# Optimization experiments

Hardware: AMD Instinct MI355X
Metric: run time of the kernel (lower is better)

The kernel has to match this reference:

```python
import jax, jax.numpy as jnp
from jax import lax
import numpy as np

NUM_KIND = 4
V, H, B = 34, 32, 4096   # raw vertical (2 rows dropped), horizontal, batch
KS = 33                  # odd-rounded max(V-2, H)
NUM_DEPTH = 4
N_SQ = 100


def _conv(x, w):
    # x: (N,1,h,w), w: (1,1,KS,KS); torch Conv2d == cross-correlation == lax default
    return lax.conv_general_dilated(x, w, (1, 1), 'SAME',
                                    dimension_numbers=('NCHW', 'OIHW', 'NCHW'))


def _conv_k(x, w):
    # x: (K,B,1,h,w) -> conv each map with the shared 1-channel kernel
    k, b, c, h, wd = x.shape
    return _conv(x.reshape(k * b, c, h, wd), w).reshape(k, b, c, h, wd)


def setup_inputs() -> dict:
    key = jax.random.key(0)
    ks = jax.random.split(key, 8)
    std = 0.3
    return {
        'dots':    jax.random.randint(ks[0], (V, H, B), 0, NUM_KIND + 1, dtype=jnp.int32),
        'w_each':  jax.random.normal(ks[1], (1, 1, KS, KS), jnp.float32) * std,
        'w_not':   jax.random.normal(ks[2], (1, 1, KS, KS), jnp.float32) * std,
        'w_not2':  jax.random.normal(ks[3], (1, 1, KS, KS), jnp.float32) * std,
        'w_empty': jax.random.normal(ks[4], (1, 1, KS, KS), jnp.float32) * std,
        'W1':      jax.random.normal(ks[5], (N_SQ, (V - 2) * H), jnp.float32) * std,
        'W2':      jax.random.normal(ks[6], (N_SQ, N_SQ), jnp.float32) * std,
        'W3':      jax.random.normal(ks[7], (1, N_SQ), jnp.float32) * std,
    }


def reference(dots, w_each, w_not, w_not2, w_empty, W1, W2, W3):
    # drop last 2 vertical rows, layout (V-2,H,B) -> (B,1,V-2,H)
    board = dots[:-2].astype(jnp.float32).transpose(2, 0, 1)[:, None]  # (B,1,h,w)

    empty = (board == 0).astype(jnp.float32)
    E = _conv(empty, w_empty)                                           # (B,1,h,w)

    kinds = jnp.arange(1, NUM_KIND + 1, dtype=board.dtype).reshape(NUM_KIND, 1, 1, 1, 1)
    each = (board[None] == kinds).astype(jnp.float32)                   # (K,B,1,h,w)
    notm = ((each + empty[None]) == 0).astype(jnp.float32)              # (K,B,1,h,w)

    # first pass: per-color value, masked to that color's cells
    notm_conv = _conv_k(notm, w_not)      # note: the torch code LOGS the convolved not-mask
    v = _conv_k(each, w_each) + E[None] - notm_conv
    L = each * v                          # each_color_value_log (masked)
    s = jax.nn.sigmoid(L.sum(axis=0))     # all_color_value_2nd, (B,1,h,w)

    # iterative diffusion; torch mutates the log in-place each depth:
    # L <- mask * (L + E + conv2nd(notm_conv * before)); before is detached
    for _ in range(NUM_DEPTH):
        before = lax.stop_gradient(s)
        C = _conv_k(notm_conv * before[None], w_not2)
        L = each * (L + E[None] + C)
        s = jax.nn.sigmoid(L.sum(axis=0))

    feat = s.reshape(s.shape[0], -1)      # (B, (V-2)*H)
    x = jax.nn.leaky_relu(feat @ W1.T, 0.2)
    x = jax.nn.leaky_relu(x @ W2.T, 0.2)
    return x @ W3.T                        # (B,1)
```

## Files before the change

kernel.cpp:

```cpp
#include <hip/hip_runtime.h>
#include <cstdint>
#include <cstddef>


typedef _Float16 f16;
typedef __attribute__((ext_vector_type(8))) _Float16 f16x8;
typedef __attribute__((ext_vector_type(4))) float f32x4;

#define NB   4096
#define PIX  1024
#define MR   (NB * 4)

__device__ __forceinline__ void gld_lds16(const void* g, void* l) {
    __builtin_amdgcn_global_load_lds(
        (const __attribute__((address_space(1))) void*)g,
        (__attribute__((address_space(3))) void*)l, 16, 0, 0);
}

__global__ void build_all(const float* __restrict__ we, const float* __restrict__ wn,
                          const float* __restrict__ wn2, const float* __restrict__ wem,
                          const float* __restrict__ W1, const int* __restrict__ dots,
                          f16* __restrict__ Me, f16* __restrict__ Mn,
                          f16* __restrict__ Mn2, f16* __restrict__ Mem,
                          f16* __restrict__ W1b, unsigned char* __restrict__ board) {
    __shared__ unsigned char tile[64][68];
    int bi = blockIdx.x, t = threadIdx.x;
    if (bi < 4096) {
        int idx = bi * 256 + t;
        int o = idx >> 10, in = idx & 1023;
        int i = o >> 5, j = o & 31, a = in >> 5, b = in & 31;
        int u = a - i + 16, v = b - j + 16;
        bool ok = (u >= 0) && (u < 33) && (v >= 0) && (v < 33);
        int w = u * 33 + v;
        float ve = 0.f, vn = 0.f, vn2 = 0.f, vem = 0.f;
        if (ok) { ve = we[w]; vn = wn[w]; vn2 = wn2[w]; vem = wem[w]; }
        Me[idx]  = (f16)ve;
        Mn[idx]  = (f16)vn;
        Mn2[idx] = (f16)vn2;
        Mem[idx] = (f16)vem;
    } else if (bi < 4608) {
        int idx = (bi - 4096) * 256 + t;
        int j = idx >> 10, i = idx & 1023;
        W1b[idx] = (f16)(j < 100 ? W1[j * 1024 + i] : 0.f);
    } else {
        int bb = bi - 4608;
        int bp = bb & 15, bn = bb >> 4;
        int p0 = bp * 64, n0 = bn * 64;
        int ln = t & 63, lp = t >> 6;
#pragma unroll
        for (int j = 0; j < 16; j++) {
            int p = lp * 16 + j;
            tile[p][ln] = (unsigned char)dots[(size_t)(p0 + p) * 4096 + n0 + ln];
        }
        __syncthreads();
#pragma unroll
        for (int j = 0; j < 16; j++) {
            int n = lp * 16 + j;
            board[(size_t)(n0 + n) * 1024 + p0 + ln] = tile[ln][n];
        }
    }
}

__global__ void mk_sa(const f16* __restrict__ S1sel, const f16* __restrict__ En,
                      const f16* __restrict__ NC,
                      const unsigned char* __restrict__ board,
                      f16* __restrict__ Lsel, f16* __restrict__ P1) {
    int idx = blockIdx.x * 256 + threadIdx.x;
    int n = idx >> 10, o = idx & 1023;
    int c = board[idx];
    size_t r0 = (size_t)(4 * n) * PIX + o;
    f16 nc0 = NC[r0], nc1 = NC[r0 + PIX], nc2 = NC[r0 + 2 * PIX], nc3 = NC[r0 + 3 * PIX];
    float L = 0.f;
    if (c > 0) {
        float ncsel = (float)((c == 1) ? nc0 : (c == 2) ? nc1 : (c == 3) ? nc2 : nc3);
        L = (float)S1sel[idx] + (float)En[idx] - ncsel;
    }
    Lsel[idx] = (f16)L;
    f16 s = (f16)(1.f / (1.f + __expf(-L)));
    P1[r0]           = nc0 * s;
    P1[r0 + PIX]     = nc1 * s;
    P1[r0 + 2 * PIX] = nc2 * s;
    P1[r0 + 3 * PIX] = nc3 * s;
}

template <int MODE, int ASRC>
__device__ __forceinline__ void run_gemm(
    int bjob, int ypx, int nx, char* smem,
    const f16* __restrict__ X, const f16* __restrict__ B,
    const unsigned char* __restrict__ board,
    f16* __restrict__ outB, int ldo) {
    char* smB = smem;
    char* smA = smem + 16384;

    const int tid = threadIdx.x;
    const int wv = tid >> 6, ln = tid & 63;
    const int wm = wv >> 1, wn_ = wv & 1;
    const int lr = ln & 15, lq = ln >> 4;

    int xcd = bjob & 7, slot = bjob >> 3;
    int bx = slot % nx;
    int by = xcd * ypx + slot / nx;
    const int rtile = by * 128, otile = bx * 128;
    const int img0 = (ASRC == 4) ? rtile : (rtile >> 2);

    const f32x4 fz = {0.f, 0.f, 0.f, 0.f};
    f32x4 acc[4][4];
#pragma unroll
    for (int i = 0; i < 4; i++)
#pragma unroll
        for (int j = 0; j < 4; j++) acc[i][j] = fz;

    for (int kb = 0; kb < 1024; kb += 64) {
#pragma unroll
        for (int t = 0; t < 4; t++) {
            int c = (wv * 4 + t) * 64 + ln;
            int row = c >> 3, gcol = (c & 7) ^ (row & 7);
            gld_lds16(B + (size_t)(otile + row) * 1024 + kb + gcol * 8, smB + c * 16);
        }
        if (ASRC == 0) {
#pragma unroll
            for (int t = 0; t < 4; t++) {
                int c = (wv * 4 + t) * 64 + ln;
                int row = c >> 3, gcol = (c & 7) ^ (row & 7);
                gld_lds16(X + (size_t)(rtile + row) * 1024 + kb + gcol * 8, smA + c * 16);
            }
        } else if (ASRC == 4) {
#pragma unroll
            for (int t = 0; t < 2; t++) {
                int c = t * 256 + wv * 64 + ln;
                int row = c >> 2, g = (c & 3) ^ (row & 3);
                gld_lds16(board + (size_t)(img0 + row) * 1024 + kb + g * 16, smA + c * 16);
            }
        } else {
            if (wv < 2) {
                int c = wv * 64 + ln;
                int row = c >> 2, g = (c & 3) ^ (row & 3);
                gld_lds16(board + (size_t)(img0 + row) * 1024 + kb + g * 16, smA + c * 16);
            }
        }
        __syncthreads();

#pragma unroll
        for (int kk = 0; kk < 2; kk++) {
            const int oct = kk * 4 + lq;
            f16x8 af[4], bfr[4];
#pragma unroll
            for (int i = 0; i < 4; i++) {
                int rrow = wm * 64 + i * 16 + lr;
                if (ASRC == 0) {
                    af[i] = *(const f16x8*)(smA + rrow * 128 + (oct ^ (rrow & 7)) * 16);
                } else {
                    int m = (ASRC == 4) ? rrow : (rrow >> 2);
                    int k1 = (rrow & 3) + 1;
                    uint64_t bb = *(const uint64_t*)(smA + m * 64 +
                                    ((oct >> 1) ^ (m & 3)) * 16 + (oct & 1) * 8);
                    f16x8 v;
#pragma unroll
                    for (int jj = 0; jj < 8; jj++) {
                        int bj = (int)((bb >> (8 * jj)) & 0xff);
                        bool on = (ASRC == 2) ? (bj == k1)
                                : (ASRC == 3) ? (bj != 0 && bj != k1)
                                              : (bj == 0);
                        v[jj] = on ? (f16)1.f : (f16)0.f;
                    }
                    af[i] = v;
                }
            }
#pragma unroll
            for (int j = 0; j < 4; j++) {
                int brow = wn_ * 64 + j * 16 + lr;
                bfr[j] = *(const f16x8*)(smB + brow * 128 + (oct ^ (brow & 7)) * 16);
            }
#pragma unroll
            for (int i = 0; i < 4; i++)
#pragma unroll
                for (int j = 0; j < 4; j++)
                    acc[i][j] = __builtin_amdgcn_mfma_f32_16x16x32_f16(
                        af[i], bfr[j], acc[i][j], 0, 0, 0);
        }
        __syncthreads();
    }

#pragma unroll
    for (int i = 0; i < 4; i++) {
        int rbase = rtile + wm * 64 + i * 16 + lq * 4;
#pragma unroll
        for (int j = 0; j < 4; j++) {
            int o = otile + wn_ * 64 + j * 16 + lr;
            f32x4 a = acc[i][j];
            if (MODE == 0) {
#pragma unroll
                for (int v = 0; v < 4; v++)
                    outB[(size_t)(rbase + v) * ldo + o] = (f16)a[v];
            } else {
                int n = rbase >> 2;
                size_t no = (size_t)n * PIX + o;
                int c = board[no];
                float asel = (c == 1) ? a[0] : (c == 2) ? a[1] : (c == 3) ? a[2] : a[3];
                outB[no] = (f16)asel;
            }
        }
    }
}

__global__ void __launch_bounds__(256, 4) gemm_fa(
    const f16* __restrict__ Me, const f16* __restrict__ Mn,
    const f16* __restrict__ Mem, const unsigned char* __restrict__ board,
    f16* __restrict__ S1sel, f16* __restrict__ NC, f16* __restrict__ En) {
    __shared__ __attribute__((aligned(16))) char smem[24576];
    int bi = blockIdx.x;
    if (bi < 1024) {
        run_gemm<1, 2>(bi, 16, 8, smem, nullptr, Me, board, S1sel, 0);
    } else if (bi < 2048) {
        run_gemm<0, 3>(bi - 1024, 16, 8, smem, nullptr, Mn, board, NC, PIX);
    } else {
        run_gemm<0, 4>(bi - 2048, 4, 8, smem, nullptr, Mem, board, En, PIX);
    }
}

template <int MODE>
__global__ void __launch_bounds__(256, 2) gemm_depth(
    const f16* __restrict__ Pin, const f16* __restrict__ Mn2,
    const unsigned char* __restrict__ board, const f16* __restrict__ NC,
    const f16* __restrict__ En, f16* __restrict__ Lsel,
    f16* __restrict__ Pout, f16* __restrict__ feat) {
    __shared__ __attribute__((aligned(16))) char smem[32768];
    char* smB = smem;
    char* smA = smem + 16384;

    const int tid = threadIdx.x;
    const int wv = tid >> 6, ln = tid & 63;
    const int wm = wv >> 1, wn_ = wv & 1;
    const int lr = ln & 15, lq = ln >> 4;

    int bi = blockIdx.x;
    int xcd = bi & 7, slot = bi >> 3;
    int bx = slot & 7;
    int by = xcd * 16 + (slot >> 3);
    const int rtile = by * 128, otile = bx * 128;

    const f32x4 fz = {0.f, 0.f, 0.f, 0.f};
    f32x4 acc[4][4];
#pragma unroll
    for (int i = 0; i < 4; i++)
#pragma unroll
        for (int j = 0; j < 4; j++) acc[i][j] = fz;

    for (int kb = 0; kb < 1024; kb += 64) {
#pragma unroll
        for (int t = 0; t < 4; t++) {
            int c = (wv * 4 + t) * 64 + ln;
            int row = c >> 3, gcol = (c & 7) ^ (row & 7);
            gld_lds16(Mn2 + (size_t)(otile + row) * 1024 + kb + gcol * 8, smB + c * 16);
            gld_lds16(Pin + (size_t)(rtile + row) * 1024 + kb + gcol * 8, smA + c * 16);
        }
        __syncthreads();

#pragma unroll
        for (int kk = 0; kk < 2; kk++) {
            const int oct = kk * 4 + lq;
            f16x8 af[4], bfr[4];
#pragma unroll
            for (int i = 0; i < 4; i++) {
                int rrow = wm * 64 + i * 16 + lr;
                af[i] = *(const f16x8*)(smA + rrow * 128 + (oct ^ (rrow & 7)) * 16);
            }
#pragma unroll
            for (int j = 0; j < 4; j++) {
                int brow = wn_ * 64 + j * 16 + lr;
                bfr[j] = *(const f16x8*)(smB + brow * 128 + (oct ^ (brow & 7)) * 16);
            }
#pragma unroll
            for (int i = 0; i < 4; i++)
#pragma unroll
                for (int j = 0; j < 4; j++)
                    acc[i][j] = __builtin_amdgcn_mfma_f32_16x16x32_f16(
                        af[i], bfr[j], acc[i][j], 0, 0, 0);
        }
        __syncthreads();
    }

#pragma unroll
    for (int i = 0; i < 4; i++) {
        int rbase = rtile + wm * 64 + i * 16 + lq * 4;
#pragma unroll
        for (int j = 0; j < 4; j++) {
            int o = otile + wn_ * 64 + j * 16 + lr;
            f32x4 a = acc[i][j];
            int n = rbase >> 2;
            size_t no = (size_t)n * PIX + o;
            int c = board[no];
            float asel = (c == 1) ? a[0] : (c == 2) ? a[1] : (c == 3) ? a[2] : a[3];
            float E = (float)En[no];
            float Lnew = (c > 0) ? ((float)Lsel[no] + E + asel) : 0.f;
            float s = 1.f / (1.f + __expf(-Lnew));
            if (MODE == 4) {
                feat[no] = (f16)s;
            } else {
                Lsel[no] = (f16)Lnew;
                f16 sh = (f16)s;
                size_t r0 = (size_t)rbase * PIX + o;
                Pout[r0]           = NC[r0] * sh;
                Pout[r0 + PIX]     = NC[r0 + PIX] * sh;
                Pout[r0 + 2 * PIX] = NC[r0 + 2 * PIX] * sh;
                Pout[r0 + 3 * PIX] = NC[r0 + 3 * PIX] * sh;
            }
        }
    }
}

__global__ void __launch_bounds__(256) gemm_mlp_fused(
    const f16* __restrict__ feat, const f16* __restrict__ W1b,
    const float* __restrict__ W2, const float* __restrict__ W3,
    float* __restrict__ out) {
    __shared__ __attribute__((aligned(16))) char smem[47360];
    char* smB = smem;
    char* smA = smem + 16384;

    const int tid = threadIdx.x;
    const int wv = tid >> 6, ln = tid & 63;
    const int wm = wv >> 1, wn_ = wv & 1;
    const int lr = ln & 15, lq = ln >> 4;
    const int rtile = blockIdx.x * 128;

    const f32x4 fz = {0.f, 0.f, 0.f, 0.f};
    f32x4 acc[4][4];
#pragma unroll
    for (int i = 0; i < 4; i++)
#pragma unroll
        for (int j = 0; j < 4; j++) acc[i][j] = fz;

    for (int kb = 0; kb < 1024; kb += 64) {
#pragma unroll
        for (int t = 0; t < 4; t++) {
            int c = (wv * 4 + t) * 64 + ln;
            int row = c >> 3, gcol = (c & 7) ^ (row & 7);
            gld_lds16(W1b  + (size_t)row * 1024 + kb + gcol * 8, smB + c * 16);
            gld_lds16(feat + (size_t)(rtile + row) * 1024 + kb + gcol * 8, smA + c * 16);
        }
        __syncthreads();
#pragma unroll
        for (int kk = 0; kk < 2; kk++) {
            const int oct = kk * 4 + lq;
            f16x8 af[4], bfr[4];
#pragma unroll
            for (int i = 0; i < 4; i++) {
                int rrow = wm * 64 + i * 16 + lr;
                af[i] = *(const f16x8*)(smA + rrow * 128 + (oct ^ (rrow & 7)) * 16);
            }
#pragma unroll
            for (int j = 0; j < 4; j++) {
                int brow = wn_ * 64 + j * 16 + lr;
                bfr[j] = *(const f16x8*)(smB + brow * 128 + (oct ^ (brow & 7)) * 16);
            }
#pragma unroll
            for (int i = 0; i < 4; i++)
#pragma unroll
                for (int j = 0; j < 4; j++)
                    acc[i][j] = __builtin_amdgcn_mfma_f32_16x16x32_f16(
                        af[i], bfr[j], acc[i][j], 0, 0, 0);
        }
        __syncthreads();
    }

    float* xs  = (float*)smem;
    f16*   sW2 = (f16*)(smem + 25856);
    float* sW3 = (float*)(smem + 45856);
    float* red = (float*)(smem + 46272);
    for (int idx = tid; idx < 10000; idx += 256) sW2[idx] = (f16)W2[idx];
    if (tid < 100) sW3[tid] = W3[tid];

    for (int half = 0; half < 2; half++) {
        if (wm == half) {
#pragma unroll
            for (int i = 0; i < 4; i++) {
                int rb = i * 16 + lq * 4;
#pragma unroll
                for (int j = 0; j < 4; j++) {
                    int o = wn_ * 64 + j * 16 + lr;
                    if (o < 100) {
                        f32x4 a = acc[i][j];
#pragma unroll
                        for (int v = 0; v < 4; v++) {
                            float x = a[v];
                            xs[(rb + v) * 101 + o] = x > 0.f ? x : 0.2f * x;
                        }
                    }
                }
            }
        }
        __syncthreads();
        int nb = tid >> 2, q = tid & 3;
        const float* xrow = xs + nb * 101;
        float partial = 0.f;
        for (int jj = 0; jj < 25; jj++) {
            int j = q + jj * 4;
            const f16* w2r = sW2 + j * 100;
            float a2 = 0.f;
#pragma unroll
            for (int i = 0; i < 100; i++) a2 += (float)w2r[i] * xrow[i];
            partial += sW3[j] * (a2 > 0.f ? a2 : 0.2f * a2);
        }
        red[tid] = partial;
        __syncthreads();
        if (q == 0)
            out[rtile + half * 64 + nb] = red[tid] + red[tid + 1] + red[tid + 2] + red[tid + 3];
        __syncthreads();
    }
}

extern "C" void kernel_launch(void* const* d_in, const int* in_sizes, int n_in,
                              void* d_out, int out_size, void* d_ws, size_t ws_size,
                              hipStream_t stream) {
    (void)in_sizes; (void)n_in; (void)out_size; (void)ws_size;
    const int*   dots   = (const int*)d_in[0];
    const float* w_each = (const float*)d_in[1];
    const float* w_not  = (const float*)d_in[2];
    const float* w_not2 = (const float*)d_in[3];
    const float* w_emp  = (const float*)d_in[4];
    const float* W1 = (const float*)d_in[5];
    const float* W2 = (const float*)d_in[6];
    const float* W3 = (const float*)d_in[7];
    float* out = (float*)d_out;

    char* ws = (char*)d_ws;
    size_t off = 0;
    auto alloc = [&](size_t bytes) -> char* {
        char* p = ws + off;
        off += (bytes + 255) & ~(size_t)255;
        return p;
    };
    f16* Me    = (f16*)alloc((size_t)PIX * PIX * 2);
    f16* Mn    = (f16*)alloc((size_t)PIX * PIX * 2);
    f16* Mn2   = (f16*)alloc((size_t)PIX * PIX * 2);
    f16* Mem   = (f16*)alloc((size_t)PIX * PIX * 2);
    f16* W1b   = (f16*)alloc((size_t)128 * PIX * 2);
    unsigned char* board = (unsigned char*)alloc((size_t)NB * PIX);
    f16* NC    = (f16*)alloc((size_t)MR * PIX * 2);
    f16* En    = (f16*)alloc((size_t)NB * PIX * 2);
    f16* S1sel = (f16*)alloc((size_t)NB * PIX * 2);
    f16* Pa    = (f16*)alloc((size_t)MR * PIX * 2);
    f16* Pb    = (f16*)alloc((size_t)MR * PIX * 2);
    f16* feat  = (f16*)alloc((size_t)NB * PIX * 2);
    f16* Lsel  = (f16*)alloc((size_t)NB * PIX * 2);

    dim3 blk(256);
    build_all<<<5632, blk, 0, stream>>>(w_each, w_not, w_not2, w_emp, W1, dots,
                                        Me, Mn, Mn2, Mem, W1b, board);
    gemm_fa<<<2304, blk, 0, stream>>>(Me, Mn, Mem, board, S1sel, NC, En);
    mk_sa<<<16384, blk, 0, stream>>>(S1sel, En, NC, board, Lsel, Pa);
    gemm_depth<3><<<1024, blk, 0, stream>>>(Pa, Mn2, board, NC, En, Lsel, Pb, nullptr);
    gemm_depth<3><<<1024, blk, 0, stream>>>(Pb, Mn2, board, NC, En, Lsel, Pa, nullptr);
    gemm_depth<3><<<1024, blk, 0, stream>>>(Pa, Mn2, board, NC, En, Lsel, Pb, nullptr);
    gemm_depth<4><<<1024, blk, 0, stream>>>(Pb, Mn2, board, NC, En, Lsel, nullptr, feat);
    gemm_mlp_fused<<<32, blk, 0, stream>>>(feat, W1b, W2, W3, out);
}
```

Baseline: 410.4 us.

## Rewrite not-mask conv as total minus each/empty convs and fuse first-pass GEMMs

The not-mask for a color is rewritten algebraically as 1 - each_k - empty, so its convolution becomes a precomputed kernel total-sum per pixel (tn) minus conv(each_k) minus conv(empty). The first-pass GEMMs are restructured so each A operand (the per-color mask or the empty mask) is loaded once and multiplied against two B matrices at the same time, which removes the separate not-mask GEMM. The result is 1280 blocks with two accumulators in place of 2304 blocks. Later kernels rebuild the not-conv values from Ek and O on the fly. This costs twice the accumulator registers (occupancy bound lowered to 2) and some extra fp16 rounding from the subtraction.

```diff
diff --git a/kernel.cpp b/kernel.cpp
--- a/kernel.cpp
+++ b/kernel.cpp
@@ -22,7 +22,8 @@
                           const float* __restrict__ W1, const int* __restrict__ dots,
                           f16* __restrict__ Me, f16* __restrict__ Mn,
                           f16* __restrict__ Mn2, f16* __restrict__ Mem,
-                          f16* __restrict__ W1b, unsigned char* __restrict__ board) {
+                          f16* __restrict__ W1b, unsigned char* __restrict__ board,
+                          float* __restrict__ tn) {
     __shared__ unsigned char tile[64][68];
     int bi = blockIdx.x, t = threadIdx.x;
     if (bi < 4096) {
@@ -42,7 +43,7 @@
         int idx = (bi - 4096) * 256 + t;
         int j = idx >> 10, i = idx & 1023;
         W1b[idx] = (f16)(j < 100 ? W1[j * 1024 + i] : 0.f);
-    } else {
+    } else if (bi < 5632) {
         int bb = bi - 4608;
         int bp = bb & 15, bn = bb >> 4;
         int p0 = bp * 64, n0 = bn * 64;
@@ -58,39 +59,54 @@
             int n = lp * 16 + j;
             board[(size_t)(n0 + n) * 1024 + p0 + ln] = tile[ln][n];
         }
+    } else {
+        int o = (bi - 5632) * 256 + t;
+        int i = o >> 5, j = o & 31;
+        int ulo = 16 - i < 0 ? 0 : 16 - i, uhi = 48 - i < 33 ? 48 - i : 33;
+        int vlo = 16 - j < 0 ? 0 : 16 - j, vhi = 48 - j < 33 ? 48 - j : 33;
+        float s = 0.f;
+        for (int u = ulo; u < uhi; u++)
+            for (int v = vlo; v < vhi; v++)
+                s += (float)(f16)wn[u * 33 + v];
+        tn[o] = s;
     }
 }
 
 __global__ void mk_sa(const f16* __restrict__ S1sel, const f16* __restrict__ En,
-                      const f16* __restrict__ NC,
+                      const f16* __restrict__ Ek, const f16* __restrict__ O,
                       const unsigned char* __restrict__ board,
                       f16* __restrict__ Lsel, f16* __restrict__ P1) {
     int idx = blockIdx.x * 256 + threadIdx.x;
     int n = idx >> 10, o = idx & 1023;
     int c = board[idx];
     size_t r0 = (size_t)(4 * n) * PIX + o;
-    f16 nc0 = NC[r0], nc1 = NC[r0 + PIX], nc2 = NC[r0 + 2 * PIX], nc3 = NC[r0 + 3 * PIX];
+    float Ov = (float)O[idx];
+    float nc0 = Ov - (float)Ek[r0];
+    float nc1 = Ov - (float)Ek[r0 + PIX];
+    float nc2 = Ov - (float)Ek[r0 + 2 * PIX];
+    float nc3 = Ov - (float)Ek[r0 + 3 * PIX];
     float L = 0.f;
     if (c > 0) {
-        float ncsel = (float)((c == 1) ? nc0 : (c == 2) ? nc1 : (c == 3) ? nc2 : nc3);
+        float ncsel = (c == 1) ? nc0 : (c == 2) ? nc1 : (c == 3) ? nc2 : nc3;
         L = (float)S1sel[idx] + (float)En[idx] - ncsel;
     }
     Lsel[idx] = (f16)L;
     f16 s = (f16)(1.f / (1.f + __expf(-L)));
-    P1[r0]           = nc0 * s;
-    P1[r0 + PIX]     = nc1 * s;
-    P1[r0 + 2 * PIX] = nc2 * s;
-    P1[r0 + 3 * PIX] = nc3 * s;
-}
-
-template <int MODE, int ASRC>
-__device__ __forceinline__ void run_gemm(
-    int bjob, int ypx, int nx, char* smem,
-    const f16* __restrict__ X, const f16* __restrict__ B,
-    const unsigned char* __restrict__ board,
-    f16* __restrict__ outB, int ldo) {
-    char* smB = smem;
-    char* smA = smem + 16384;
+    P1[r0]           = (f16)nc0 * s;
+    P1[r0 + PIX]     = (f16)nc1 * s;
+    P1[r0 + 2 * PIX] = (f16)nc2 * s;
+    P1[r0 + 3 * PIX] = (f16)nc3 * s;
+}
+
+template <int JOB>
+__device__ __forceinline__ void run_fa2(
+    int bjob, int ypx, char* smem,
+    const f16* __restrict__ B1, const f16* __restrict__ B2,
+    const unsigned char* __restrict__ board, const float* __restrict__ tn,
+    f16* __restrict__ out1, f16* __restrict__ out2) {
+    char* smB1 = smem;
+    char* smB2 = smem + 16384;
+    char* smA  = smem + 32768;
 
     const int tid = threadIdx.x;
     const int wv = tid >> 6, ln = tid & 63;
@@ -98,33 +114,28 @@
     const int lr = ln & 15, lq = ln >> 4;
 
     int xcd = bjob & 7, slot = bjob >> 3;
-    int bx = slot % nx;
-    int by = xcd * ypx + slot / nx;
+    int bx = slot & 7;
+    int by = xcd * ypx + (slot >> 3);
     const int rtile = by * 128, otile = bx * 128;
-    const int img0 = (ASRC == 4) ? rtile : (rtile >> 2);
+    const int img0 = (JOB == 2) ? rtile : (rtile >> 2);
 
     const f32x4 fz = {0.f, 0.f, 0.f, 0.f};
-    f32x4 acc[4][4];
+    f32x4 acc1[4][4], acc2[4][4];
 #pragma unroll
     for (int i = 0; i < 4; i++)
 #pragma unroll
-        for (int j = 0; j < 4; j++) acc[i][j] = fz;
+        for (int j = 0; j < 4; j++) { acc1[i][j] = fz; acc2[i][j] = fz; }
 
     for (int kb = 0; kb < 1024; kb += 64) {
 #pragma unroll
         for (int t = 0; t < 4; t++) {
             int c = (wv * 4 + t) * 64 + ln;
             int row = c >> 3, gcol = (c & 7) ^ (row & 7);
-            gld_lds16(B + (size_t)(otile + row) * 1024 + kb + gcol * 8, smB + c * 16);
-        }
-        if (ASRC == 0) {
-#pragma unroll
-            for (int t = 0; t < 4; t++) {
-                int c = (wv * 4 + t) * 64 + ln;
-                int row = c >> 3, gcol = (c & 7) ^ (row & 7);
-                gld_lds16(X + (size_t)(rtile + row) * 1024 + kb + gcol * 8, smA + c * 16);
-            }
-        } else if (ASRC == 4) {
+            size_t goff = (size_t)(otile + row) * 1024 + kb + gcol * 8;
+            gld_lds16(B1 + goff, smB1 + c * 16);
+            gld_lds16(B2 + goff, smB2 + c * 16);
+        }
+        if (JOB == 2) {
 #pragma unroll
             for (int t = 0; t < 2; t++) {
                 int c = t * 256 + wv * 64 + ln;
@@ -143,40 +154,39 @@
 #pragma unroll
         for (int kk = 0; kk < 2; kk++) {
             const int oct = kk * 4 + lq;
-            f16x8 af[4], bfr[4];
+            f16x8 af[4], bf1[4], bf2[4];
 #pragma unroll
             for (int i = 0; i < 4; i++) {
                 int rrow = wm * 64 + i * 16 + lr;
-                if (ASRC == 0) {
-                    af[i] = *(const f16x8*)(smA + rrow * 128 + (oct ^ (rrow & 7)) * 16);
-                } else {
-                    int m = (ASRC == 4) ? rrow : (rrow >> 2);
-                    int k1 = (rrow & 3) + 1;
-                    uint64_t bb = *(const uint64_t*)(smA + m * 64 +
-                                    ((oct >> 1) ^ (m & 3)) * 16 + (oct & 1) * 8);
-                    f16x8 v;
-#pragma unroll
-                    for (int jj = 0; jj < 8; jj++) {
-                        int bj = (int)((bb >> (8 * jj)) & 0xff);
-                        bool on = (ASRC == 2) ? (bj == k1)
-                                : (ASRC == 3) ? (bj != 0 && bj != k1)
-                                              : (bj == 0);
-                        v[jj] = on ? (f16)1.f : (f16)0.f;
-                    }
-                    af[i] = v;
+                int m = (JOB == 2) ? rrow : (rrow >> 2);
+                int k1 = (rrow & 3) + 1;
+                uint64_t bb = *(const uint64_t*)(smA + m * 64 +
+                                ((oct >> 1) ^ (m & 3)) * 16 + (oct & 1) * 8);
+                f16x8 v;
+#pragma unroll
+                for (int jj = 0; jj < 8; jj++) {
+                    int bj = (int)((bb >> (8 * jj)) & 0xff);
+                    bool on = (JOB == 2) ? (bj == 0) : (bj == k1);
+                    v[jj] = on ? (f16)1.f : (f16)0.f;
                 }
+                af[i] = v;
             }
 #pragma unroll
             for (int j = 0; j < 4; j++) {
                 int brow = wn_ * 64 + j * 16 + lr;
-                bfr[j] = *(const f16x8*)(smB + brow * 128 + (oct ^ (brow & 7)) * 16);
+                int boff = brow * 128 + (oct ^ (brow & 7)) * 16;
+                bf1[j] = *(const f16x8*)(smB1 + boff);
+                bf2[j] = *(const f16x8*)(smB2 + boff);
             }
 #pragma unroll
             for (int i = 0; i < 4; i++)
 #pragma unroll
-                for (int j = 0; j < 4; j++)
-                    acc[i][j] = __builtin_amdgcn_mfma_f32_16x16x32_f16(
-                        af[i], bfr[j], acc[i][j], 0, 0, 0);
+                for (int j = 0; j < 4; j++) {
+                    acc1[i][j] = __builtin_amdgcn_mfma_f32_16x16x32_f16(
+                        af[i], bf1[j], acc1[i][j], 0, 0, 0);
+                    acc2[i][j] = __builtin_amdgcn_mfma_f32_16x16x32_f16(
+                        af[i], bf2[j], acc2[i][j], 0, 0, 0);
+                }
         }
         __syncthreads();
     }
@@ -187,43 +197,51 @@
 #pragma unroll
         for (int j = 0; j < 4; j++) {
             int o = otile + wn_ * 64 + j * 16 + lr;
-            f32x4 a = acc[i][j];
-            if (MODE == 0) {
-#pragma unroll
-                for (int v = 0; v < 4; v++)
-                    outB[(size_t)(rbase + v) * ldo + o] = (f16)a[v];
-            } else {
+            f32x4 a1 = acc1[i][j], a2 = acc2[i][j];
+            if (JOB == 1) {
                 int n = rbase >> 2;
                 size_t no = (size_t)n * PIX + o;
                 int c = board[no];
-                float asel = (c == 1) ? a[0] : (c == 2) ? a[1] : (c == 3) ? a[2] : a[3];
-                outB[no] = (f16)asel;
-            }
-        }
-    }
-}
-
-__global__ void __launch_bounds__(256, 4) gemm_fa(
+                float asel = (c == 1) ? a1[0] : (c == 2) ? a1[1]
+                           : (c == 3) ? a1[2] : a1[3];
+                out1[no] = (f16)asel;
+                size_t r0 = (size_t)rbase * PIX + o;
+#pragma unroll
+                for (int v = 0; v < 4; v++)
+                    out2[r0 + (size_t)v * PIX] = (f16)a2[v];
+            } else {
+                float tno = tn[o];
+#pragma unroll
+                for (int v = 0; v < 4; v++) {
+                    size_t no = (size_t)(rbase + v) * PIX + o;
+                    out1[no] = (f16)a1[v];
+                    out2[no] = (f16)(tno - a2[v]);
+                }
+            }
+        }
+    }
+}
+
+__global__ void __launch_bounds__(256, 2) gemm_fa2(
     const f16* __restrict__ Me, const f16* __restrict__ Mn,
     const f16* __restrict__ Mem, const unsigned char* __restrict__ board,
-    f16* __restrict__ S1sel, f16* __restrict__ NC, f16* __restrict__ En) {
-    __shared__ __attribute__((aligned(16))) char smem[24576];
+    const float* __restrict__ tn, f16* __restrict__ S1sel,
+    f16* __restrict__ Ek, f16* __restrict__ En, f16* __restrict__ O) {
+    __shared__ __attribute__((aligned(16))) char smem[40960];
     int bi = blockIdx.x;
     if (bi < 1024) {
-        run_gemm<1, 2>(bi, 16, 8, smem, nullptr, Me, board, S1sel, 0);
-    } else if (bi < 2048) {
-        run_gemm<0, 3>(bi - 1024, 16, 8, smem, nullptr, Mn, board, NC, PIX);
+        run_fa2<1>(bi, 16, smem, Me, Mn, board, tn, S1sel, Ek);
     } else {
-        run_gemm<0, 4>(bi - 2048, 4, 8, smem, nullptr, Mem, board, En, PIX);
+        run_fa2<2>(bi - 1024, 4, smem, Mem, Mn, board, tn, En, O);
     }
 }
 
 template <int MODE>
 __global__ void __launch_bounds__(256, 2) gemm_depth(
     const f16* __restrict__ Pin, const f16* __restrict__ Mn2,
-    const unsigned char* __restrict__ board, const f16* __restrict__ NC,
-    const f16* __restrict__ En, f16* __restrict__ Lsel,
-    f16* __restrict__ Pout, f16* __restrict__ feat) {
+    const unsigned char* __restrict__ board, const f16* __restrict__ Ek,
+    const f16* __restrict__ O, const f16* __restrict__ En,
+    f16* __restrict__ Lsel, f16* __restrict__ Pout, f16* __restrict__ feat) {
     __shared__ __attribute__((aligned(16))) char smem[32768];
     char* smB = smem;
     char* smA = smem + 16384;
@@ -298,12 +316,12 @@
                 feat[no] = (f16)s;
             } else {
                 Lsel[no] = (f16)Lnew;
-                f16 sh = (f16)s;
+                float Ov = (float)O[no];
                 size_t r0 = (size_t)rbase * PIX + o;
-                Pout[r0]           = NC[r0] * sh;
-                Pout[r0 + PIX]     = NC[r0 + PIX] * sh;
-                Pout[r0 + 2 * PIX] = NC[r0 + 2 * PIX] * sh;
-                Pout[r0 + 3 * PIX] = NC[r0 + 3 * PIX] * sh;
+                Pout[r0]           = (f16)((Ov - (float)Ek[r0]) * s);
+                Pout[r0 + PIX]     = (f16)((Ov - (float)Ek[r0 + PIX]) * s);
+                Pout[r0 + 2 * PIX] = (f16)((Ov - (float)Ek[r0 + 2 * PIX]) * s);
+                Pout[r0 + 3 * PIX] = (f16)((Ov - (float)Ek[r0 + 3 * PIX]) * s);
             }
         }
     }
@@ -436,22 +454,24 @@
     f16* Mem   = (f16*)alloc((size_t)PIX * PIX * 2);
     f16* W1b   = (f16*)alloc((size_t)128 * PIX * 2);
     unsigned char* board = (unsigned char*)alloc((size_t)NB * PIX);
-    f16* NC    = (f16*)alloc((size_t)MR * PIX * 2);
+    f16* Ek    = (f16*)alloc((size_t)MR * PIX * 2);
+    f16* O     = (f16*)alloc((size_t)NB * PIX * 2);
     f16* En    = (f16*)alloc((size_t)NB * PIX * 2);
     f16* S1sel = (f16*)alloc((size_t)NB * PIX * 2);
     f16* Pa    = (f16*)alloc((size_t)MR * PIX * 2);
     f16* Pb    = (f16*)alloc((size_t)MR * PIX * 2);
     f16* feat  = (f16*)alloc((size_t)NB * PIX * 2);
     f16* Lsel  = (f16*)alloc((size_t)NB * PIX * 2);
+    float* tn  = (float*)alloc((size_t)PIX * 4);
 
     dim3 blk(256);
-    build_all<<<5632, blk, 0, stream>>>(w_each, w_not, w_not2, w_emp, W1, dots,
-                                        Me, Mn, Mn2, Mem, W1b, board);
-    gemm_fa<<<2304, blk, 0, stream>>>(Me, Mn, Mem, board, S1sel, NC, En);
-    mk_sa<<<16384, blk, 0, stream>>>(S1sel, En, NC, board, Lsel, Pa);
-    gemm_depth<3><<<1024, blk, 0, stream>>>(Pa, Mn2, board, NC, En, Lsel, Pb, nullptr);
-    gemm_depth<3><<<1024, blk, 0, stream>>>(Pb, Mn2, board, NC, En, Lsel, Pa, nullptr);
-    gemm_depth<3><<<1024, blk, 0, stream>>>(Pa, Mn2, board, NC, En, Lsel, Pb, nullptr);
-    gemm_depth<4><<<1024, blk, 0, stream>>>(Pb, Mn2, board, NC, En, Lsel, nullptr, feat);
+    build_all<<<5636, blk, 0, stream>>>(w_each, w_not, w_not2, w_emp, W1, dots,
+                                        Me, Mn, Mn2, Mem, W1b, board, tn);
+    gemm_fa2<<<1280, blk, 0, stream>>>(Me, Mn, Mem, board, tn, S1sel, Ek, En, O);
+    mk_sa<<<16384, blk, 0, stream>>>(S1sel, En, Ek, O, board, Lsel, Pa);
+    gemm_depth<3><<<1024, blk, 0, stream>>>(Pa, Mn2, board, Ek, O, En, Lsel, Pb, nullptr);
+    gemm_depth<3><<<1024, blk, 0, stream>>>(Pb, Mn2, board, Ek, O, En, Lsel, Pa, nullptr);
+    gemm_depth<3><<<1024, blk, 0, stream>>>(Pa, Mn2, board, Ek, O, En, Lsel, Pb, nullptr);
+    gemm_depth<4><<<1024, blk, 0, stream>>>(Pb, Mn2, board, Ek, O, En, Lsel, nullptr, feat);
     gemm_mlp_fused<<<32, blk, 0, stream>>>(feat, W1b, W2, W3, out);
 }
```

Measured after the change: 502.0 us. +22.3%, slower.
